# Optimization experiments

Measured on AMD Instinct MI355X. Metric: run time of the kernel, lower is better.

## Reference

```python
import jax, jax.numpy as jnp
import numpy as np

NUM_HEADS = 8

def dwconv(x, w, b, pad):
    # depthwise conv: x [B, C, H, W], w [C, 1, k, k], groups=C
    y = jax.lax.conv_general_dilated(
        x, w, window_strides=(1, 1), padding=[(pad, pad), (pad, pad)],
        feature_group_count=x.shape[1], dimension_numbers=('NCHW', 'OIHW', 'NCHW'))
    return y + b[None, :, None, None]


def setup_inputs() -> dict:
    key = jax.random.key(0)
    ks = jax.random.split(key, 12)
    B, H, W = 32, 28, 28
    C = 512
    N = 1 + H * W
    Ch = C // NUM_HEADS  # 64
    s = lambda k, shp, fan: jax.random.normal(k, shp, jnp.float32) * (fan ** -0.5)
    return {
        'x': jax.random.normal(ks[0], (B, N, C), jnp.float32),
        'qkv_w': s(ks[1], (3 * C, C), C),
        'qkv_b': jnp.zeros((3 * C,), jnp.float32),
        'proj_w': s(ks[2], (C, C), C),
        'proj_b': jnp.zeros((C,), jnp.float32),
        'w3': s(ks[3], (2 * Ch, 1, 3, 3), 9),
        'b3': jnp.zeros((2 * Ch,), jnp.float32),
        'w5': s(ks[4], (3 * Ch, 1, 5, 5), 25),
        'b5': jnp.zeros((3 * Ch,), jnp.float32),
        'w7': s(ks[5], (3 * Ch, 1, 7, 7), 49),
        'b7': jnp.zeros((3 * Ch,), jnp.float32),
        'H': H,
        'W': W,
    }


def reference(x, qkv_w, qkv_b, proj_w, proj_b, w3, b3, w5, b5, w7, b7, H, W):
    B, N, C = x.shape
    h = NUM_HEADS
    Ch = C // h
    scale = Ch ** -0.5
    # qkv projection -> q, k, v each [B, h, N, Ch]
    qkv = (x @ qkv_w.T + qkv_b).reshape(B, N, 3, h, Ch).transpose(2, 0, 3, 1, 4)
    q, k, v = qkv[0], qkv[1], qkv[2]
    # factorized attention: softmax over tokens on k, then (k^T v) then q @ ...
    k_sm = jax.nn.softmax(k, axis=2)
    kv = jnp.einsum('bhnc,bhnd->bhcd', k_sm, v)          # [B,h,Ch,Ch]
    factor_att = jnp.einsum('bhnc,bhcd->bhnd', q, kv)    # [B,h,N,Ch]
    # conv relative position encoding (CRPE) on image tokens only
    q_img = q[:, :, 1:, :]                               # [B,h,HW,Ch]
    v_img = v[:, :, 1:, :].transpose(0, 1, 3, 2).reshape(B, h * Ch, H, W)
    splits = np.cumsum([2 * Ch, 3 * Ch, 3 * Ch])[:-1]
    v1, v2, v3 = jnp.split(v_img, splits, axis=1)
    conv_v = jnp.concatenate(
        [dwconv(v1, w3, b3, 1), dwconv(v2, w5, b5, 2), dwconv(v3, w7, b7, 3)], axis=1)
    conv_v = conv_v.reshape(B, h, Ch, H * W).transpose(0, 1, 3, 2)  # [B,h,HW,Ch]
    EV = q_img * conv_v
    crpe = jnp.pad(EV, ((0, 0), (0, 0), (1, 0), (0, 0)))  # zero row for cls token
    out = scale * factor_att + crpe
    out = out.transpose(0, 2, 1, 3).reshape(B, N, C)
    return out @ proj_w.T + proj_b
```

## Files before the change

kernel.cpp:

```cpp
#include <hip/hip_runtime.h>
#include <cstdint>
#include <cstddef>


typedef unsigned short u16;

#define HEADS 8
#define CHD   64
#define CDIM  512
#define NTOK  785
#define BATCH 32
#define MROWS (BATCH * NTOK)
#define MPAD  25344
#define QKVN  1536
#define IMGHW 784

typedef float  f32x4  __attribute__((ext_vector_type(4)));
typedef __bf16 bf16x8 __attribute__((ext_vector_type(8)));

__device__ __forceinline__ u16 f2bf(float f) {
  union { float f; uint32_t u; } x; x.f = f;
  uint32_t r = x.u + 0x7fffu + ((x.u >> 16) & 1u);
  return (u16)(r >> 16);
}
__device__ __forceinline__ float bf2f(u16 u) {
  union { uint32_t u; float f; } x; x.u = ((uint32_t)u) << 16;
  return x.f;
}
__device__ __forceinline__ float bflo(uint32_t u) { return bf2f((u16)(u & 0xffffu)); }
__device__ __forceinline__ float bfhi(uint32_t u) { return bf2f((u16)(u >> 16)); }
__device__ __forceinline__ uint32_t pk2(float a, float b) {
#if __has_builtin(__builtin_amdgcn_cvt_pk_bf16_f32)
  auto v = __builtin_amdgcn_cvt_pk_bf16_f32(a, b);
  union { decltype(v) v2; uint32_t u; } cv; cv.v2 = v; return cv.u;
#else
  return (uint32_t)f2bf(a) | ((uint32_t)f2bf(b) << 16);
#endif
}

__global__ __launch_bounds__(256)
void casts_kernel(const float* __restrict__ x, u16* __restrict__ xb,
                  const float* __restrict__ w1, u16* __restrict__ w1b,
                  const float* __restrict__ w2, u16* __restrict__ w2b) {
  const int N1 = MROWS * CDIM / 4, N2 = QKVN * CDIM / 4, N3 = CDIM * CDIM / 4;
  int i = blockIdx.x * 256 + threadIdx.x;
  const float* src; u16* dst;
  if (i < N1)           { src = x;  dst = xb;  }
  else if (i < N1 + N2) { i -= N1;  src = w1; dst = w1b; }
  else if (i < N1 + N2 + N3) { i -= N1 + N2; src = w2; dst = w2b; }
  else return;
  float4 v = reinterpret_cast<const float4*>(src)[i];
  uint2 o; o.x = pk2(v.x, v.y); o.y = pk2(v.z, v.w);
  reinterpret_cast<uint2*>(dst)[i] = o;
}

__device__ __forceinline__ void gld_lds16(const u16* g, u16* l) {
  __builtin_amdgcn_global_load_lds((__attribute__((address_space(1))) void*)g,
                                   (__attribute__((address_space(3))) void*)l,
                                   16, 0, 0);
}

template <int OUTBF16>
__global__ __launch_bounds__(512)
void gemm_bt(const u16* __restrict__ A, const u16* __restrict__ W,
             const float* __restrict__ bias, void* __restrict__ Cout,
             int Mstore, int N, int K, int nMt, int nNt) {
  __shared__ __align__(16) u16 lsA[2][256 * 32];
  __shared__ __align__(16) u16 lsB[2][128 * 32];
  const int flat = blockIdx.x;
  const int xcd = flat & 7, idx = flat >> 3;
  const int nt = idx % nNt;
  const int mt = (idx / nNt) * 8 + xcd;
  if (mt >= nMt) return;
  const int tile_m = mt * 256, tile_n = nt * 128;

  const int tid  = threadIdx.x;
  const int wave = tid >> 6, lane = tid & 63;
  const int quad = lane >> 4, l16 = lane & 15;
  const int wm = (wave & 3) * 64, wn = (wave >> 2) * 64;

  const int srow = tid >> 2;
  const int scol = ((tid & 3) ^ ((tid >> 3) & 3)) * 8;
  const int ldst = tid * 8;

  auto stage = [&](int kt, int buf) {
    const int kc = kt * 32 + scol;
#pragma unroll
    for (int s = 0; s < 2; ++s)
      gld_lds16(A + (size_t)(tile_m + s * 128 + srow) * K + kc,
                &lsA[buf][s * 4096 + ldst]);
    gld_lds16(W + (size_t)(tile_n + srow) * K + kc, &lsB[buf][ldst]);
  };

  f32x4 acc[4][4] = {};

  stage(0, 0);
  __syncthreads();

  const int KT = K >> 5;
  const int pch = (quad ^ ((l16 >> 1) & 3)) * 8;
#pragma unroll 2
  for (int t = 0; t < KT; ++t) {
    const int cur = t & 1;
    if (t + 1 < KT) stage(t + 1, cur ^ 1);
    bf16x8 af[4], bfr[4];
#pragma unroll
    for (int i = 0; i < 4; ++i) {
      af[i]  = *reinterpret_cast<const bf16x8*>(
          &lsA[cur][(wm + i * 16 + l16) * 32 + pch]);
      bfr[i] = *reinterpret_cast<const bf16x8*>(
          &lsB[cur][(wn + i * 16 + l16) * 32 + pch]);
    }
#pragma unroll
    for (int i = 0; i < 4; ++i)
#pragma unroll
      for (int j = 0; j < 4; ++j)
        acc[i][j] = __builtin_amdgcn_mfma_f32_16x16x32_bf16(
            af[i], bfr[j], acc[i][j], 0, 0, 0);
    __syncthreads();
  }

#pragma unroll
  for (int i = 0; i < 4; ++i) {
    const int mbase = tile_m + wm + i * 16 + quad * 4;
#pragma unroll
    for (int j = 0; j < 4; ++j) {
      const int n  = tile_n + wn + j * 16 + l16;
      const float bv = bias[n];
      const float v0 = acc[i][j][0] + bv, v1 = acc[i][j][1] + bv;
      const float v2 = acc[i][j][2] + bv, v3 = acc[i][j][3] + bv;
      if (OUTBF16) {
        u16* cp = reinterpret_cast<u16*>(Cout) + (size_t)mbase * N + n;
        const uint32_t p01 = pk2(v0, v1), p23 = pk2(v2, v3);
        if (mbase + 0 < Mstore) cp[0]            = (u16)p01;
        if (mbase + 1 < Mstore) cp[(size_t)N]    = (u16)(p01 >> 16);
        if (mbase + 2 < Mstore) cp[(size_t)N*2]  = (u16)p23;
        if (mbase + 3 < Mstore) cp[(size_t)N*3]  = (u16)(p23 >> 16);
      } else {
        float* cp = reinterpret_cast<float*>(Cout) + (size_t)mbase * N + n;
        if (mbase + 0 < Mstore) cp[0]           = v0;
        if (mbase + 1 < Mstore) cp[(size_t)N]   = v1;
        if (mbase + 2 < Mstore) cp[(size_t)N*2] = v2;
        if (mbase + 3 < Mstore) cp[(size_t)N*3] = v3;
      }
    }
  }
}

__device__ __forceinline__ void kv_part(
    const u16* __restrict__ qkv, u16* __restrict__ kvT, int bh,
    float* __restrict__ e_s, float* __restrict__ v_s) {
  const int b = bh >> 3, h = bh & 7;
  const int t = threadIdx.x;
  const int c4 = (t & 15) * 4;
  const int d4 = (t >> 4) * 4;
  const u16* kbase = qkv + (size_t)(b * NTOK) * QKVN + CDIM + h * CHD;
  const u16* vbase = kbase + CDIM;
  f32x4 acc[4] = {};
  f32x4 sp4 = {0.f, 0.f, 0.f, 0.f};

  for (int n0 = 0; n0 < NTOK; n0 += 32) {
    const int nc = min(32, NTOK - n0);
    __syncthreads();
    for (int i4 = t; i4 < nc * 16; i4 += 256) {
      const int nl = i4 >> 4;
      const uint2 kk = *reinterpret_cast<const uint2*>(
          &kbase[(size_t)(n0 + nl) * QKVN + c4]);
      const uint2 vv = *reinterpret_cast<const uint2*>(
          &vbase[(size_t)(n0 + nl) * QKVN + c4]);
      f32x4 e4, v4;
      e4[0] = __expf(bflo(kk.x)); e4[1] = __expf(bfhi(kk.x));
      e4[2] = __expf(bflo(kk.y)); e4[3] = __expf(bfhi(kk.y));
      v4[0] = bflo(vv.x); v4[1] = bfhi(vv.x);
      v4[2] = bflo(vv.y); v4[3] = bfhi(vv.y);
      *reinterpret_cast<f32x4*>(&e_s[nl * 64 + c4]) = e4;
      *reinterpret_cast<f32x4*>(&v_s[nl * 64 + c4]) = v4;
      sp4 += e4;
    }
    __syncthreads();
    for (int nl = 0; nl < nc; ++nl) {
      const f32x4 e4 = *reinterpret_cast<const f32x4*>(&e_s[nl * 64 + c4]);
      const f32x4 v4 = *reinterpret_cast<const f32x4*>(&v_s[nl * 64 + d4]);
      acc[0] += e4[0] * v4;
      acc[1] += e4[1] * v4;
      acc[2] += e4[2] * v4;
      acc[3] += e4[3] * v4;
    }
  }
  __syncthreads();
  *reinterpret_cast<f32x4*>(&e_s[t * 4]) = sp4;
  __syncthreads();
  if (t < 64) {
    float S = 0.f;
#pragma unroll
    for (int m = 0; m < 16; ++m)
      S += e_s[((t >> 2) + 16 * m) * 4 + (t & 3)];
    v_s[t] = S;
  }
  __syncthreads();
  const float S0 = v_s[c4], S1 = v_s[c4 + 1], S2 = v_s[c4 + 2], S3 = v_s[c4 + 3];
  u16* kb = kvT + (size_t)bh * 4096 + (size_t)d4 * 64 + c4;
#pragma unroll
  for (int di = 0; di < 4; ++di) {
    uint2 o;
    o.x = pk2(acc[0][di] / S0, acc[1][di] / S1);
    o.y = pk2(acc[2][di] / S2, acc[3][di] / S3);
    *reinterpret_cast<uint2*>(&kb[(size_t)di * 64]) = o;
  }
}

template <int KS>
__device__ __forceinline__ void conv_head(
    const u16* __restrict__ qkv, const float* __restrict__ wgt,
    const float* __restrict__ bias, int b, int head, int hh, int yt,
    u16* __restrict__ evbuf, u16* __restrict__ ls, float* __restrict__ wls) {
  constexpr int PAD = KS / 2;
  constexpr int RIN = 4 + 2 * PAD;
  const int t = threadIdx.x;
  const int y0 = yt * 4;
  const u16* vimg = qkv + (size_t)(b * NTOK + 1) * QKVN + 2 * CDIM + head * 64;
  for (int i = t; i < 64 * KS * KS; i += 256)
    wls[i] = wgt[hh * 64 * KS * KS + i];
  const int c8 = (t & 7) * 8;
  for (int pi = t >> 3; pi < RIN * 28; pi += 32) {
    const int ry = pi / 28, rx = pi - ry * 28;
    const int yy = y0 - PAD + ry;
    uint4 val = {0, 0, 0, 0};
    if (yy >= 0 && yy < 28)
      val = *reinterpret_cast<const uint4*>(vimg + (size_t)(yy * 28 + rx) * QKVN + c8);
    *reinterpret_cast<uint4*>(ls + pi * 64 + c8) = val;
  }
  __syncthreads();
  const int d = t & 63, yl = t >> 6;
  float wr[KS * KS];
#pragma unroll
  for (int i = 0; i < KS * KS; ++i) wr[i] = wls[d * KS * KS + i];
  const float bv = bias[hh * 64 + d];
  float acc[28];
#pragma unroll
  for (int x = 0; x < 28; ++x) acc[x] = bv;
#pragma unroll
  for (int xx = 0; xx < 28; ++xx) {
    float col[KS];
#pragma unroll
    for (int r = 0; r < KS; ++r)
      col[r] = bf2f(ls[((yl + r) * 28 + xx) * 64 + d]);
#pragma unroll
    for (int j = 0; j < KS; ++j) {
      const int x = xx + PAD - j;
      if (x >= 0 && x < 28) {
#pragma unroll
        for (int r = 0; r < KS; ++r)
          acc[x] += col[r] * wr[r * KS + j];
      }
    }
  }
  const int p0 = (y0 + yl) * 28;
  const u16* qrow = qkv + (size_t)(b * NTOK + 1 + p0) * QKVN + head * 64 + d;
  u16* obase = evbuf + (((size_t)(b * 8 + head)) * IMGHW + p0) * 64 + d;
#pragma unroll
  for (int x = 0; x < 28; ++x) {
    const float ev = acc[x] * bf2f(qrow[(size_t)x * QKVN]);
    obase[(size_t)x * 64] = f2bf(ev);
  }
}

__global__ __launch_bounds__(256)
void kv_conv_kernel(const u16* __restrict__ qkv, u16* __restrict__ kvT,
                    const float* __restrict__ w3, const float* __restrict__ b3,
                    const float* __restrict__ w5, const float* __restrict__ b5,
                    const float* __restrict__ w7, const float* __restrict__ b7,
                    u16* __restrict__ evbuf) {
  __shared__ __align__(16) char smem[10 * 28 * 64 * 2 + 64 * 49 * 4];
  const int y = blockIdx.y;
  if (y == 0) {
    float* e_s = reinterpret_cast<float*>(smem);
    float* v_s = e_s + 32 * 64;
    kv_part(qkv, kvT, blockIdx.x, e_s, v_s);
  } else {
    u16* ls = reinterpret_cast<u16*>(smem);
    float* wls = reinterpret_cast<float*>(smem + 10 * 28 * 64 * 2);
    const int b = blockIdx.x >> 3, h = blockIdx.x & 7, yt = y - 1;
    if (h < 2)      conv_head<3>(qkv, w3, b3, b, h, h,     yt, evbuf, ls, wls);
    else if (h < 5) conv_head<5>(qkv, w5, b5, b, h, h - 2, yt, evbuf, ls, wls);
    else            conv_head<7>(qkv, w7, b7, b, h, h - 5, yt, evbuf, ls, wls);
  }
}

__global__ __launch_bounds__(256)
void combine_kernel(const u16* __restrict__ qkv, const u16* __restrict__ kvT,
                    const u16* __restrict__ evbuf, u16* __restrict__ attn) {
  __shared__ __align__(16) float sa[128 * 64];
  const int bh = blockIdx.x;
  const int b = bh >> 3, h = bh & 7;
  const int t = threadIdx.x;
  const int wave = t >> 6, lane = t & 63;
  const int quad = lane >> 4, l16 = lane & 15;
  const int tokbase = blockIdx.y * 256 + wave * 64;

  const u16* kvb = kvT + (size_t)bh * 4096;
  bf16x8 bfr[4][2];
#pragma unroll
  for (int j = 0; j < 4; ++j)
#pragma unroll
    for (int kk = 0; kk < 2; ++kk)
      bfr[j][kk] = *reinterpret_cast<const bf16x8*>(
          &kvb[(j * 16 + l16) * 64 + kk * 32 + quad * 8]);

  bf16x8 af[4][2];
#pragma unroll
  for (int i = 0; i < 4; ++i) {
    const int tok = min(tokbase + i * 16 + l16, NTOK - 1);
    const u16* qrow = qkv + (size_t)(b * NTOK + tok) * QKVN + h * CHD;
    af[i][0] = *reinterpret_cast<const bf16x8*>(&qrow[quad * 8]);
    af[i][1] = *reinterpret_cast<const bf16x8*>(&qrow[32 + quad * 8]);
  }

  f32x4 acc[4][4] = {};
#pragma unroll
  for (int kk = 0; kk < 2; ++kk)
#pragma unroll
    for (int i = 0; i < 4; ++i)
#pragma unroll
      for (int j = 0; j < 4; ++j)
        acc[i][j] = __builtin_amdgcn_mfma_f32_16x16x32_bf16(af[i][kk], bfr[j][kk], acc[i][j], 0, 0, 0);

  const float scale = 0.125f;
  const u16* evb = evbuf + (size_t)bh * IMGHW * 64;
#pragma unroll
  for (int half = 0; half < 2; ++half) {
    if ((wave >> 1) == half) {
      const int rbase = (wave & 1) * 64;
#pragma unroll
      for (int i = 0; i < 4; ++i)
#pragma unroll
        for (int rr = 0; rr < 4; ++rr) {
          const int rl = rbase + i * 16 + quad * 4 + rr;
#pragma unroll
          for (int j = 0; j < 4; ++j) {
            const int dd = j * 16 + l16;
            sa[rl * 64 + (((dd >> 2) ^ (rl & 15)) * 4) + (dd & 3)] =
                scale * acc[i][j][rr];
          }
        }
    }
    __syncthreads();
    {
      const int rl = t >> 1;
      const int tok = blockIdx.y * 256 + half * 128 + rl;
      if (tok < NTOK) {
        u16* orow = attn + (size_t)(b * NTOK + tok) * CDIM + h * CHD;
        const int cb = (t & 1) * 8;
#pragma unroll
        for (int c2 = 0; c2 < 4; ++c2) {
          const int ch0 = cb + c2 * 2;
          const f32x4 v0 = *reinterpret_cast<const f32x4*>(
              &sa[rl * 64 + ((ch0 ^ (rl & 15)) * 4)]);
          const f32x4 v1 = *reinterpret_cast<const f32x4*>(
              &sa[rl * 64 + (((ch0 + 1) ^ (rl & 15)) * 4)]);
          float o0 = v0[0], o1 = v0[1], o2 = v0[2], o3 = v0[3];
          float o4 = v1[0], o5 = v1[1], o6 = v1[2], o7 = v1[3];
          if (tok > 0) {
            const uint4 ev = *reinterpret_cast<const uint4*>(
                &evb[(size_t)(tok - 1) * 64 + ch0 * 4]);
            o0 += bflo(ev.x); o1 += bfhi(ev.x);
            o2 += bflo(ev.y); o3 += bfhi(ev.y);
            o4 += bflo(ev.z); o5 += bfhi(ev.z);
            o6 += bflo(ev.w); o7 += bfhi(ev.w);
          }
          uint4 ow;
          ow.x = pk2(o0, o1); ow.y = pk2(o2, o3);
          ow.z = pk2(o4, o5); ow.w = pk2(o6, o7);
          *reinterpret_cast<uint4*>(&orow[ch0 * 4]) = ow;
        }
      }
    }
    __syncthreads();
  }
}

extern "C" void kernel_launch(void* const* d_in, const int* in_sizes, int n_in,
                              void* d_out, int out_size, void* d_ws, size_t ws_size,
                              hipStream_t stream) {
  const float* x      = (const float*)d_in[0];
  const float* qkv_w  = (const float*)d_in[1];
  const float* qkv_b  = (const float*)d_in[2];
  const float* proj_w = (const float*)d_in[3];
  const float* proj_b = (const float*)d_in[4];
  const float* w3 = (const float*)d_in[5];
  const float* b3 = (const float*)d_in[6];
  const float* w5 = (const float*)d_in[7];
  const float* b5 = (const float*)d_in[8];
  const float* w7 = (const float*)d_in[9];
  const float* b7 = (const float*)d_in[10];
  float* out = (float*)d_out;

  char* p = (char*)d_ws;
  u16* xb    = (u16*)p;   p += (size_t)MPAD * CDIM * 2;
  u16* wqb   = (u16*)p;   p += (size_t)QKVN * CDIM * 2;
  u16* wpb   = (u16*)p;   p += (size_t)CDIM * CDIM * 2;
  u16* qkvb  = (u16*)p;   p += (size_t)MPAD * QKVN * 2;
  u16* kvT   = (u16*)p;   p += (size_t)256 * 64 * 64 * 2;
  u16* attn  = (u16*)p;   p += (size_t)MPAD * CDIM * 2;
  u16* evbuf = xb;

  {
    const int total = MROWS * CDIM / 4 + QKVN * CDIM / 4 + CDIM * CDIM / 4;
    casts_kernel<<<(total + 255) / 256, 256, 0, stream>>>(x, xb, qkv_w, wqb, proj_w, wpb);
  }
  gemm_bt<1><<<13 * 8 * 12, 512, 0, stream>>>(xb, wqb, qkv_b, qkvb,
                                              MPAD, QKVN, CDIM, 99, 12);
  kv_conv_kernel<<<dim3(256, 8), 256, 0, stream>>>(
      qkvb, kvT, w3, b3, w5, b5, w7, b7, evbuf);
  combine_kernel<<<dim3(256, 4), 256, 0, stream>>>(qkvb, kvT, evbuf, attn);
  gemm_bt<0><<<13 * 8 * 4, 512, 0, stream>>>(attn, wpb, proj_b, out,
                                             MROWS, CDIM, CDIM, 99, 4);
}
```

Measured before the change: 295.2 us.

## Prefetch K/V into registers and double-buffer LDS in kv_part

The kv_part token loop now loads the next 32-token chunk of K and V into registers while the current chunk is being accumulated. It stores the chunks into two alternating LDS buffers, which drops one __syncthreads per chunk. The aim is to hide global-load latency behind the outer-product accumulation. In exchange it uses more registers and twice the LDS for this path, which still fits in the shared allocation made for the conv path.

```diff
diff --git a/kernel.cpp b/kernel.cpp
--- a/kernel.cpp
+++ b/kernel.cpp
@@ -154,33 +154,55 @@
   const int t = threadIdx.x;
   const int c4 = (t & 15) * 4;
   const int d4 = (t >> 4) * 4;
+  const int nl0 = t >> 4;
   const u16* kbase = qkv + (size_t)(b * NTOK) * QKVN + CDIM + h * CHD;
   const u16* vbase = kbase + CDIM;
   f32x4 acc[4] = {};
   f32x4 sp4 = {0.f, 0.f, 0.f, 0.f};
 
-  for (int n0 = 0; n0 < NTOK; n0 += 32) {
-    const int nc = min(32, NTOK - n0);
+  const int NCH = (NTOK + 31) / 32;
+  uint2 rk0, rv0, rk1, rv1;
+  auto issue = [&](int c) {
+    const int na = c * 32 + nl0, nb = na + 16;
+    if (na < NTOK) {
+      rk0 = *reinterpret_cast<const uint2*>(&kbase[(size_t)na * QKVN + c4]);
+      rv0 = *reinterpret_cast<const uint2*>(&vbase[(size_t)na * QKVN + c4]);
+    }
+    if (nb < NTOK) {
+      rk1 = *reinterpret_cast<const uint2*>(&kbase[(size_t)nb * QKVN + c4]);
+      rv1 = *reinterpret_cast<const uint2*>(&vbase[(size_t)nb * QKVN + c4]);
+    }
+  };
+
+  issue(0);
+  for (int c = 0; c < NCH; ++c) {
+    float* eb = e_s + (c & 1) * 2048;
+    float* vb = v_s + (c & 1) * 2048;
+    const int na = c * 32 + nl0, nb = na + 16;
+    f32x4 e4a = {}, v4a = {}, e4b = {}, v4b = {};
+    if (na < NTOK) {
+      e4a[0] = __expf(bflo(rk0.x)); e4a[1] = __expf(bfhi(rk0.x));
+      e4a[2] = __expf(bflo(rk0.y)); e4a[3] = __expf(bfhi(rk0.y));
+      v4a[0] = bflo(rv0.x); v4a[1] = bfhi(rv0.x);
+      v4a[2] = bflo(rv0.y); v4a[3] = bfhi(rv0.y);
+    }
+    if (nb < NTOK) {
+      e4b[0] = __expf(bflo(rk1.x)); e4b[1] = __expf(bfhi(rk1.x));
+      e4b[2] = __expf(bflo(rk1.y)); e4b[3] = __expf(bfhi(rk1.y));
+      v4b[0] = bflo(rv1.x); v4b[1] = bfhi(rv1.x);
+      v4b[2] = bflo(rv1.y); v4b[3] = bfhi(rv1.y);
+    }
+    *reinterpret_cast<f32x4*>(&eb[nl0 * 64 + c4]) = e4a;
+    *reinterpret_cast<f32x4*>(&vb[nl0 * 64 + c4]) = v4a;
+    *reinterpret_cast<f32x4*>(&eb[(nl0 + 16) * 64 + c4]) = e4b;
+    *reinterpret_cast<f32x4*>(&vb[(nl0 + 16) * 64 + c4]) = v4b;
+    sp4 += e4a + e4b;
+    if (c + 1 < NCH) issue(c + 1);
     __syncthreads();
-    for (int i4 = t; i4 < nc * 16; i4 += 256) {
-      const int nl = i4 >> 4;
-      const uint2 kk = *reinterpret_cast<const uint2*>(
-          &kbase[(size_t)(n0 + nl) * QKVN + c4]);
-      const uint2 vv = *reinterpret_cast<const uint2*>(
-          &vbase[(size_t)(n0 + nl) * QKVN + c4]);
-      f32x4 e4, v4;
-      e4[0] = __expf(bflo(kk.x)); e4[1] = __expf(bfhi(kk.x));
-      e4[2] = __expf(bflo(kk.y)); e4[3] = __expf(bfhi(kk.y));
-      v4[0] = bflo(vv.x); v4[1] = bfhi(vv.x);
-      v4[2] = bflo(vv.y); v4[3] = bfhi(vv.y);
-      *reinterpret_cast<f32x4*>(&e_s[nl * 64 + c4]) = e4;
-      *reinterpret_cast<f32x4*>(&v_s[nl * 64 + c4]) = v4;
-      sp4 += e4;
-    }
-    __syncthreads();
+    const int nc = min(32, NTOK - c * 32);
     for (int nl = 0; nl < nc; ++nl) {
-      const f32x4 e4 = *reinterpret_cast<const f32x4*>(&e_s[nl * 64 + c4]);
-      const f32x4 v4 = *reinterpret_cast<const f32x4*>(&v_s[nl * 64 + d4]);
+      const f32x4 e4 = *reinterpret_cast<const f32x4*>(&eb[nl * 64 + c4]);
+      const f32x4 v4 = *reinterpret_cast<const f32x4*>(&vb[nl * 64 + d4]);
       acc[0] += e4[0] * v4;
       acc[1] += e4[1] * v4;
       acc[2] += e4[2] * v4;
@@ -275,7 +297,7 @@
   const int y = blockIdx.y;
   if (y == 0) {
     float* e_s = reinterpret_cast<float*>(smem);
-    float* v_s = e_s + 32 * 64;
+    float* v_s = e_s + 2 * 2048;
     kv_part(qkv, kvT, blockIdx.x, e_s, v_s);
   } else {
     u16* ls = reinterpret_cast<u16*>(smem);
```

Result: no change. 293.5 us (-0.6%).
